# Optimization experiments

Hardware: AMD Instinct MI355X
Metric: run time of the kernel (lower is better)

Reference implementation:

```python
import jax, jax.numpy as jnp
import numpy as np

N = 50000
E = 1600000
SI, SO, VI, VO, H, SVOD = 128, 128, 16, 16, 16, 3
EPS = 1e-8


def _safe_norm(x, axis, keepdims=False):
    return jnp.sqrt(jnp.sum(x * x, axis=axis, keepdims=keepdims) + EPS)


def setup_inputs() -> dict:
    key = jax.random.key(0)
    ks = jax.random.split(key, 13)

    def lin(k, fan_in, shape):
        b = 1.0 / np.sqrt(fan_in)
        return jax.random.uniform(k, shape, jnp.float32, -b, b)

    merged_dim = H + SI + 3 * SVOD  # 153
    return {
        "s": jax.random.normal(ks[0], (N, SI), jnp.float32),
        "v": jax.random.normal(ks[1], (N, VI, 3), jnp.float32),
        "frames": jax.random.normal(ks[2], (E, 3, 3), jnp.float32),
        "W_vd": lin(ks[3], VI, (VI, H)),            # vector_down (no bias)
        "W_vdf": lin(ks[4], VI, (VI, SVOD)),        # vector_down_frames (no bias)
        "W_so": lin(ks[5], merged_dim, (merged_dim, SO)),  # scalar_out
        "b_so": lin(ks[6], merged_dim, (SO,)),
        "W_vu": lin(ks[7], H, (H, VO)),             # vector_up (no bias)
        "W_vosf": lin(ks[8], SO, (SO, 3 * SVOD)),   # vector_out_scale_frames
        "b_vosf": lin(ks[9], SO, (3 * SVOD,)),
        "W_vuf": lin(ks[10], SVOD, (SVOD, VO)),     # vector_up_frames (no bias)
        "edge_index": jax.random.randint(ks[11], (2, E), 0, N, jnp.int32),
        "node_inputs": 1,
    }


def reference(s, v, frames, W_vd, W_vdf, W_so, b_so, W_vu, W_vosf, b_vosf, W_vuf, edge_index, node_inputs):
    # node_inputs is assumed truthy (node-wise GCP): gather by source node, scatter-mean back.
    row = edge_index[0]
    deg = jax.ops.segment_sum(jnp.ones((E,), s.dtype), row, num_segments=N)
    inv_deg = 1.0 / jnp.maximum(deg, 1.0)

    v_pre = jnp.swapaxes(v, -1, -2)                 # [N, 3, VI]
    vh = v_pre @ W_vd                                # [N, 3, H]
    vnorm = _safe_norm(vh, axis=-2)                  # [N, H]
    vdf = v_pre @ W_vdf                              # [N, 3, SVOD]

    # scalarize: project gathered source-node vectors onto per-edge frames, scatter-mean
    local = jnp.einsum('eij,ejc->eic', frames, vdf[row])       # [E, 3, SVOD]
    local9 = jnp.swapaxes(local, -1, -2).reshape(E, 3 * SVOD)  # [E, 9]
    sh = jax.ops.segment_sum(local9, row, num_segments=N) * inv_deg[:, None]  # [N, 9]

    merged = jnp.concatenate([s, vnorm, sh], axis=-1)          # [N, SI+H+9]
    scalar_rep = merged @ W_so + b_so                           # [N, SO]

    # vector path with frame gate
    vr = jnp.swapaxes(vh @ W_vu, -1, -2)                        # [N, VO, 3]
    gate = jax.nn.sigmoid(scalar_rep) @ W_vosf + b_vosf         # [N, 9]
    # vectorize: expand gate scalars back into vectors via frames, scatter-mean
    g = gate[row].reshape(E, 3, 3)
    gv_e = jnp.einsum('eji,ejk->eik', g, frames)                # [E, 3, 3]
    gv = jax.ops.segment_sum(gv_e, row, num_segments=N) * inv_deg[:, None, None]  # [N, 3, 3]
    gvr = jnp.swapaxes(jnp.swapaxes(gv, -1, -2) @ W_vuf, -1, -2)  # [N, VO, 3]
    vr = vr * jax.nn.sigmoid(_safe_norm(gvr, axis=-1, keepdims=True))

    return jax.nn.relu(scalar_rep), vr
```

## Files before the change

kernel.cpp:

```cpp
#include <hip/hip_runtime.h>

#define N_NODES 50000
#define N_EDGES 1600000
#define NPB     16
#define NCHAIN  16
#define KSTR    168
#define EPSV    1e-8f

typedef float f32x4 __attribute__((ext_vector_type(4)));
typedef short s16x8 __attribute__((ext_vector_type(8)));

struct f4u { float a, b, c, d; };

__device__ __forceinline__ float sigmoidf_(float x) { return 1.0f / (1.0f + __expf(-x)); }
__device__ __forceinline__ short f2bf(float x) {
    unsigned u = __float_as_uint(x);
    unsigned r = (u + 0x7FFFu + ((u >> 16) & 1u)) >> 16;
    return (short)r;
}
__device__ __forceinline__ float bf2f(short h) {
    return __uint_as_float(((unsigned)(unsigned short)h) << 16);
}

__global__ __launch_bounds__(256) void init_kernel(
    const float* __restrict__ W_so, short* __restrict__ WThi, short* __restrict__ WTlo,
    int* __restrict__ head) {
    int i = blockIdx.x * 256 + threadIdx.x;
    if (i < 128 * 160) {
        int o = i / 160, k = i - o * 160;
        float w = (k < 153) ? W_so[k * 128 + o] : 0.0f;
        short hh = f2bf(w);
        WThi[i] = hh;
        WTlo[i] = f2bf(w - bf2f(hh));
    }
    if (i < N_NODES * NCHAIN) head[i] = -1;
}

__global__ __launch_bounds__(256) void bucket_fat_kernel(
    const int* __restrict__ row,
    const float* __restrict__ frames,
    int* __restrict__ head,
    float* __restrict__ pay) {
    int e = blockIdx.x * 256 + threadIdx.x;
    if (e >= N_EDGES) return;
    int r = row[e];
    int prev = atomicExch(&head[r * NCHAIN + (e & (NCHAIN - 1))], e);
    const float* f = frames + (size_t)e * 9;
    const f4u* fp = (const f4u*)f;
    f4u x = fp[0];
    f4u y = fp[1];
    float z8 = f[8];
    float4* dst = (float4*)(pay + (size_t)e * 16);
    dst[0] = make_float4(x.a, x.b, x.c, x.d);
    dst[1] = make_float4(y.a, y.b, y.c, y.d);
    dst[2] = make_float4(z8, __int_as_float(prev), 0.0f, 0.0f);
}

__global__ __launch_bounds__(256) void bucket_thin_kernel(
    const int* __restrict__ row,
    int* __restrict__ head,
    int* __restrict__ nxt) {
    int e = blockIdx.x * 256 + threadIdx.x;
    if (e >= N_EDGES) return;
    int r = row[e];
    int prev = atomicExch(&head[r * NCHAIN + (e & (NCHAIN - 1))], e);
    nxt[e] = prev;
}

template<int FAT>
__global__ __launch_bounds__(256) void node_kernel(
    const float* __restrict__ s,
    const float* __restrict__ v,
    const float* __restrict__ fr,
    const float* __restrict__ W_vd,
    const float* __restrict__ W_vdf,
    const short* __restrict__ WThi,
    const short* __restrict__ WTlo,
    const float* __restrict__ b_so,
    const float* __restrict__ W_vu,
    const float* __restrict__ W_vosf,
    const float* __restrict__ b_vosf,
    const float* __restrict__ W_vuf,
    const int* __restrict__ head,
    const int* __restrict__ nxt,
    float* __restrict__ out0,
    float* __restrict__ out1)
{
    __shared__ __align__(16) short AL[2][NPB][KSTR];
    __shared__ float vL[NPB][48];
    __shared__ float vhL[NPB][3][16];
    __shared__ float FbarL[NPB][9];
    __shared__ float gateL[NPB][12];

    float (*sigL)[128] = (float (*)[128])&AL[0][0][0];

    const int t = threadIdx.x;
    const int base = blockIdx.x * NPB;
    const int nn = t >> 4, h = t & 15;
    const int n = base + nn;

    int e = head[(size_t)n * NCHAIN + h];

#pragma unroll
    for (int r = 0; r < 3; r++) vL[nn][h * 3 + r] = v[(size_t)n * 48 + h * 3 + r];
    {
        const float4* sp4 = (const float4*)(s + (size_t)n * 128 + h * 8);
        float4 s0 = sp4[0], s1 = sp4[1];
        float sv[8] = {s0.x, s0.y, s0.z, s0.w, s1.x, s1.y, s1.z, s1.w};
        s16x8 shi, slo;
#pragma unroll
        for (int j = 0; j < 8; j++) {
            short hh = f2bf(sv[j]);
            shi[j] = hh;
            slo[j] = f2bf(sv[j] - bf2f(hh));
        }
        *(s16x8*)&AL[0][nn][h * 8] = shi;
        *(s16x8*)&AL[1][nn][h * 8] = slo;
    }

    float fs[10];
#pragma unroll
    for (int k = 0; k < 10; k++) fs[k] = 0.f;
    {
        if (FAT) {
            while (e >= 0) {
                const float4* p = (const float4*)(fr + (size_t)e * 16);
                float4 c2 = p[2];
                float4 c0 = p[0];
                float4 c1 = p[1];
                int en = __float_as_int(c2.y);
                fs[0] += c0.x; fs[1] += c0.y; fs[2] += c0.z; fs[3] += c0.w;
                fs[4] += c1.x; fs[5] += c1.y; fs[6] += c1.z; fs[7] += c1.w;
                fs[8] += c2.x;
                fs[9] += 1.0f;
                e = en;
            }
        } else {
            while (e >= 0) {
                int en = nxt[e];
                const float* f = fr + (size_t)e * 9;
                const f4u* fp = (const f4u*)f;
                f4u x = fp[0];
                f4u y = fp[1];
                float z8 = f[8];
                fs[0] += x.a; fs[1] += x.b; fs[2] += x.c; fs[3] += x.d;
                fs[4] += y.a; fs[5] += y.b; fs[6] += y.c; fs[7] += y.d;
                fs[8] += z8;
                fs[9] += 1.0f;
                e = en;
            }
        }
#pragma unroll
        for (int m = 1; m < 16; m <<= 1) {
#pragma unroll
            for (int k = 0; k < 10; k++) fs[k] += __shfl_xor(fs[k], m);
        }
        if (h < 9) {
            float inv = 1.0f / fmaxf(fs[9], 1.0f);
            FbarL[nn][h] = fs[h] * inv;
        }
    }
    __syncthreads();

    {
        float vh0 = 0.f, vh1 = 0.f, vh2 = 0.f;
#pragma unroll
        for (int i = 0; i < 16; i++) {
            float w = W_vd[i * 16 + h];
            vh0 += vL[nn][i * 3 + 0] * w;
            vh1 += vL[nn][i * 3 + 1] * w;
            vh2 += vL[nn][i * 3 + 2] * w;
        }
        vhL[nn][0][h] = vh0; vhL[nn][1][h] = vh1; vhL[nn][2][h] = vh2;
        float vn = sqrtf(vh0 * vh0 + vh1 * vh1 + vh2 * vh2 + EPSV);
        short hh = f2bf(vn);
        AL[0][nn][128 + h] = hh;
        AL[1][nn][128 + h] = f2bf(vn - bf2f(hh));
        if (h < 9) {
            const int c = h / 3, i = h % 3;
            const float inv = 1.0f / fmaxf(fs[9], 1.0f);
            float a = 0.f;
#pragma unroll
            for (int j = 0; j < 3; j++) {
                float vd = 0.f;
#pragma unroll
                for (int ii = 0; ii < 16; ii++) vd += vL[nn][ii * 3 + j] * W_vdf[ii * 3 + c];
                a += (fs[i * 3 + j] * inv) * vd;
            }
            short hs = f2bf(a);
            AL[0][nn][144 + h] = hs;
            AL[1][nn][144 + h] = f2bf(a - bf2f(hs));
        } else {
            AL[0][nn][144 + h] = 0;
            AL[1][nn][144 + h] = 0;
        }
    }
    __syncthreads();

    {
        const int w = t >> 6;
        const int lane = t & 63;
        const int quad = lane >> 4;
        const int col = lane & 15;
        const int o0 = w * 32 + col, o1 = o0 + 16;
        f32x4 acc0 = (f32x4){0.f, 0.f, 0.f, 0.f};
        f32x4 acc1 = (f32x4){0.f, 0.f, 0.f, 0.f};
#pragma unroll
        for (int kk = 0; kk < 5; kk++) {
            const int krow = kk * 32 + quad * 8;
            s16x8 ahi = *(const s16x8*)&AL[0][col][krow];
            s16x8 alo = *(const s16x8*)&AL[1][col][krow];
            s16x8 b0h = *(const s16x8*)&WThi[o0 * 160 + krow];
            s16x8 b0l = *(const s16x8*)&WTlo[o0 * 160 + krow];
            s16x8 b1h = *(const s16x8*)&WThi[o1 * 160 + krow];
            s16x8 b1l = *(const s16x8*)&WTlo[o1 * 160 + krow];
            acc0 = __builtin_amdgcn_mfma_f32_16x16x32_bf16(ahi, b0h, acc0, 0, 0, 0);
            acc0 = __builtin_amdgcn_mfma_f32_16x16x32_bf16(ahi, b0l, acc0, 0, 0, 0);
            acc0 = __builtin_amdgcn_mfma_f32_16x16x32_bf16(alo, b0h, acc0, 0, 0, 0);
            acc1 = __builtin_amdgcn_mfma_f32_16x16x32_bf16(ahi, b1h, acc1, 0, 0, 0);
            acc1 = __builtin_amdgcn_mfma_f32_16x16x32_bf16(ahi, b1l, acc1, 0, 0, 0);
            acc1 = __builtin_amdgcn_mfma_f32_16x16x32_bf16(alo, b1h, acc1, 0, 0, 0);
        }
        __syncthreads();
        {
            float b0 = b_so[o0], b1 = b_so[o1];
#pragma unroll
            for (int r = 0; r < 4; r++) {
                int nl = quad * 4 + r;
                float v0 = acc0[r] + b0;
                float v1 = acc1[r] + b1;
                out0[(size_t)(base + nl) * 128 + o0] = fmaxf(v0, 0.0f);
                out0[(size_t)(base + nl) * 128 + o1] = fmaxf(v1, 0.0f);
                sigL[nl][o0] = sigmoidf_(v0);
                sigL[nl][o1] = sigmoidf_(v1);
            }
        }
    }
    __syncthreads();

    {
        const float* sp = &sigL[nn][h * 8];
        float4 s0 = *(const float4*)sp;
        float4 s1 = *(const float4*)(sp + 4);
        float sv[8] = {s0.x, s0.y, s0.z, s0.w, s1.x, s1.y, s1.z, s1.w};
        float p[9];
#pragma unroll
        for (int k = 0; k < 9; k++) p[k] = 0.f;
#pragma unroll
        for (int i = 0; i < 8; i++) {
            int o = h * 8 + i;
#pragma unroll
            for (int k = 0; k < 9; k++) p[k] += sv[i] * W_vosf[o * 9 + k];
        }
#pragma unroll
        for (int m = 1; m < 16; m <<= 1) {
#pragma unroll
            for (int k = 0; k < 9; k++) p[k] += __shfl_xor(p[k], m);
        }
        if (h < 9) gateL[nn][h] = p[h] + b_vosf[h];
    }
    __syncthreads();

    {
        int o = h;
        float gv[9];
#pragma unroll
        for (int i = 0; i < 3; i++)
#pragma unroll
            for (int kk = 0; kk < 3; kk++) {
                float a = 0.f;
#pragma unroll
                for (int j = 0; j < 3; j++) a += gateL[nn][j * 3 + i] * FbarL[nn][j * 3 + kk];
                gv[i * 3 + kk] = a;
            }
        float gvr[3];
#pragma unroll
        for (int kk = 0; kk < 3; kk++) {
            float a = 0.f;
#pragma unroll
            for (int i = 0; i < 3; i++) a += gv[i * 3 + kk] * W_vuf[i * 16 + o];
            gvr[kk] = a;
        }
        float gn2 = sqrtf(gvr[0] * gvr[0] + gvr[1] * gvr[1] + gvr[2] * gvr[2] + EPSV);
        float sg = sigmoidf_(gn2);
#pragma unroll
        for (int c = 0; c < 3; c++) {
            float a = 0.f;
#pragma unroll
            for (int h2 = 0; h2 < 16; h2++) a += vhL[nn][c][h2] * W_vu[h2 * 16 + o];
            out1[(size_t)n * 48 + o * 3 + c] = a * sg;
        }
    }
}

extern "C" void kernel_launch(void* const* d_in, const int* in_sizes, int n_in,
                              void* d_out, int out_size, void* d_ws, size_t ws_size,
                              hipStream_t stream) {
    const float* s      = (const float*)d_in[0];
    const float* v      = (const float*)d_in[1];
    const float* frames = (const float*)d_in[2];
    const float* W_vd   = (const float*)d_in[3];
    const float* W_vdf  = (const float*)d_in[4];
    const float* W_so   = (const float*)d_in[5];
    const float* b_so   = (const float*)d_in[6];
    const float* W_vu   = (const float*)d_in[7];
    const float* W_vosf = (const float*)d_in[8];
    const float* b_vosf = (const float*)d_in[9];
    const float* W_vuf  = (const float*)d_in[10];
    const int* edge_index = (const int*)d_in[11];

    const size_t head_b = (size_t)N_NODES * NCHAIN * sizeof(int);
    const size_t wt_b   = (size_t)128 * 160 * sizeof(short);
    const size_t pay_off = head_b + 2 * wt_b;
    int*   head = (int*)d_ws;
    short* WThi = (short*)((char*)d_ws + head_b);
    short* WTlo = WThi + 128 * 160;
    float* out0 = (float*)d_out;
    float* out1 = out0 + (size_t)N_NODES * 128;

    const size_t fat_need = pay_off + (size_t)N_EDGES * 64;
    init_kernel<<<(N_NODES * NCHAIN + 255) / 256, 256, 0, stream>>>(W_so, WThi, WTlo, head);

    if (ws_size >= fat_need) {
        float* pay = (float*)((char*)d_ws + pay_off);
        bucket_fat_kernel<<<(N_EDGES + 255) / 256, 256, 0, stream>>>(edge_index, frames, head, pay);
        node_kernel<1><<<N_NODES / NPB, 256, 0, stream>>>(
            s, v, pay, W_vd, W_vdf, WThi, WTlo, b_so, W_vu, W_vosf, b_vosf, W_vuf,
            head, (const int*)nullptr, out0, out1);
    } else {
        int* nxt = (int*)((char*)d_ws + pay_off);
        bucket_thin_kernel<<<(N_EDGES + 255) / 256, 256, 0, stream>>>(edge_index, head, nxt);
        node_kernel<0><<<N_NODES / NPB, 256, 0, stream>>>(
            s, v, frames, W_vd, W_vdf, WThi, WTlo, b_so, W_vu, W_vosf, b_vosf, W_vuf,
            head, nxt, out0, out1);
    }
}
```

Measured before the change: 279.6 us.

## Bucket edge frames into per-node fixed-capacity slots instead of linked chains

Adds a CSR-like bucketing path: each edge atomically claims a slot in a per-node array of capacity up to 64 and writes its 9 frame values there. Edges beyond capacity fall back to linked-list chains. The node kernel then reads slots with coalesced strided access instead of serial pointer chasing, and derives the degree from the counter. This removes dependent-load latency in the aggregation, at the cost of a more contended per-node atomic counter and a larger padded workspace.

Result: slower. 307.5 us (+10.0%).

```diff
diff --git a/kernel.cpp b/kernel.cpp
--- a/kernel.cpp
+++ b/kernel.cpp
@@ -24,7 +24,7 @@
 
 __global__ __launch_bounds__(256) void init_kernel(
     const float* __restrict__ W_so, short* __restrict__ WThi, short* __restrict__ WTlo,
-    int* __restrict__ head) {
+    int* __restrict__ p0, int* __restrict__ p1, int mode) {
     int i = blockIdx.x * 256 + threadIdx.x;
     if (i < 128 * 160) {
         int o = i / 160, k = i - o * 160;
@@ -33,7 +33,39 @@
         WThi[i] = hh;
         WTlo[i] = f2bf(w - bf2f(hh));
     }
-    if (i < N_NODES * NCHAIN) head[i] = -1;
+    if (mode == 2) {
+        if (i < N_NODES) p0[i] = 0;
+        if (i < N_NODES * NCHAIN) p1[i] = -1;
+    } else {
+        if (i < N_NODES * NCHAIN) p0[i] = -1;
+    }
+}
+
+__global__ __launch_bounds__(256) void bucket_csr_kernel(
+    const int* __restrict__ row,
+    const float* __restrict__ frames,
+    int* __restrict__ cnt,
+    int* __restrict__ head2,
+    int* __restrict__ nxt_ovf,
+    float* __restrict__ pay,
+    int cap) {
+    int e = blockIdx.x * 256 + threadIdx.x;
+    if (e >= N_EDGES) return;
+    int r = row[e];
+    int lidx = atomicAdd(&cnt[r], 1);
+    if (lidx < cap) {
+        const float* f = frames + (size_t)e * 9;
+        f4u x = ((const f4u*)f)[0];
+        f4u y = ((const f4u*)f)[1];
+        float z8 = f[8];
+        float* dst = pay + ((size_t)r * cap + lidx) * 12;
+        *(float4*)dst       = make_float4(x.a, x.b, x.c, x.d);
+        *(float4*)(dst + 4) = make_float4(y.a, y.b, y.c, y.d);
+        *(float4*)(dst + 8) = make_float4(z8, 0.0f, 0.0f, 0.0f);
+    } else {
+        int prev = atomicExch(&head2[r * NCHAIN + (e & (NCHAIN - 1))], e);
+        nxt_ovf[e] = prev;
+    }
 }
 
 __global__ __launch_bounds__(256) void bucket_fat_kernel(
@@ -46,9 +78,8 @@
     int r = row[e];
     int prev = atomicExch(&head[r * NCHAIN + (e & (NCHAIN - 1))], e);
     const float* f = frames + (size_t)e * 9;
-    const f4u* fp = (const f4u*)f;
-    f4u x = fp[0];
-    f4u y = fp[1];
+    f4u x = ((const f4u*)f)[0];
+    f4u y = ((const f4u*)f)[1];
     float z8 = f[8];
     float4* dst = (float4*)(pay + (size_t)e * 16);
     dst[0] = make_float4(x.a, x.b, x.c, x.d);
@@ -67,11 +98,12 @@
     nxt[e] = prev;
 }
 
-template<int FAT>
+template<int MODE>
 __global__ __launch_bounds__(256) void node_kernel(
     const float* __restrict__ s,
     const float* __restrict__ v,
     const float* __restrict__ fr,
+    const float* __restrict__ frames_raw,
     const float* __restrict__ W_vd,
     const float* __restrict__ W_vdf,
     const short* __restrict__ WThi,
@@ -81,8 +113,10 @@
     const float* __restrict__ W_vosf,
     const float* __restrict__ b_vosf,
     const float* __restrict__ W_vuf,
-    const int* __restrict__ head,
+    const int* __restrict__ cnt_or_head,
+    const int* __restrict__ head2,
     const int* __restrict__ nxt,
+    int cap,
     float* __restrict__ out0,
     float* __restrict__ out1)
 {
@@ -99,7 +133,9 @@
     const int nn = t >> 4, h = t & 15;
     const int n = base + nn;
 
-    int e = head[(size_t)n * NCHAIN + h];
+    int e0;
+    if (MODE == 2) e0 = cnt_or_head[n];
+    else           e0 = cnt_or_head[(size_t)n * NCHAIN + h];
 
 #pragma unroll
     for (int r = 0; r < 3; r++) vL[nn][h * 3 + r] = v[(size_t)n * 48 + h * 3 + r];
@@ -121,8 +157,40 @@
     float fs[10];
 #pragma unroll
     for (int k = 0; k < 10; k++) fs[k] = 0.f;
-    {
-        if (FAT) {
+    float invdeg;
+    {
+        if (MODE == 2) {
+            const int cn = e0;
+            const int lim = cn < cap ? cn : cap;
+            for (int slot = h; slot < lim; slot += 16) {
+                const float* pp = fr + ((size_t)n * cap + slot) * 12;
+                float4 c0 = *(const float4*)pp;
+                float4 c1 = *(const float4*)(pp + 4);
+                float f8 = pp[8];
+                fs[0] += c0.x; fs[1] += c0.y; fs[2] += c0.z; fs[3] += c0.w;
+                fs[4] += c1.x; fs[5] += c1.y; fs[6] += c1.z; fs[7] += c1.w;
+                fs[8] += f8;
+            }
+            int e2 = head2[(size_t)n * NCHAIN + h];
+            while (e2 >= 0) {
+                int en = nxt[e2];
+                const float* f = frames_raw + (size_t)e2 * 9;
+                f4u x = ((const f4u*)f)[0];
+                f4u y = ((const f4u*)f)[1];
+                float z8 = f[8];
+                fs[0] += x.a; fs[1] += x.b; fs[2] += x.c; fs[3] += x.d;
+                fs[4] += y.a; fs[5] += y.b; fs[6] += y.c; fs[7] += y.d;
+                fs[8] += z8;
+                e2 = en;
+            }
+#pragma unroll
+            for (int m = 1; m < 16; m <<= 1) {
+#pragma unroll
+                for (int k = 0; k < 9; k++) fs[k] += __shfl_xor(fs[k], m);
+            }
+            invdeg = 1.0f / fmaxf((float)cn, 1.0f);
+        } else if (MODE == 1) {
+            int e = e0;
             while (e >= 0) {
                 const float4* p = (const float4*)(fr + (size_t)e * 16);
                 float4 c2 = p[2];
@@ -135,13 +203,19 @@
                 fs[9] += 1.0f;
                 e = en;
             }
+#pragma unroll
+            for (int m = 1; m < 16; m <<= 1) {
+#pragma unroll
+                for (int k = 0; k < 10; k++) fs[k] += __shfl_xor(fs[k], m);
+            }
+            invdeg = 1.0f / fmaxf(fs[9], 1.0f);
         } else {
+            int e = e0;
             while (e >= 0) {
                 int en = nxt[e];
                 const float* f = fr + (size_t)e * 9;
-                const f4u* fp = (const f4u*)f;
-                f4u x = fp[0];
-                f4u y = fp[1];
+                f4u x = ((const f4u*)f)[0];
+                f4u y = ((const f4u*)f)[1];
                 float z8 = f[8];
                 fs[0] += x.a; fs[1] += x.b; fs[2] += x.c; fs[3] += x.d;
                 fs[4] += y.a; fs[5] += y.b; fs[6] += y.c; fs[7] += y.d;
@@ -149,16 +223,14 @@
                 fs[9] += 1.0f;
                 e = en;
             }
-        }
-#pragma unroll
-        for (int m = 1; m < 16; m <<= 1) {
-#pragma unroll
-            for (int k = 0; k < 10; k++) fs[k] += __shfl_xor(fs[k], m);
-        }
-        if (h < 9) {
-            float inv = 1.0f / fmaxf(fs[9], 1.0f);
-            FbarL[nn][h] = fs[h] * inv;
-        }
+#pragma unroll
+            for (int m = 1; m < 16; m <<= 1) {
+#pragma unroll
+                for (int k = 0; k < 10; k++) fs[k] += __shfl_xor(fs[k], m);
+            }
+            invdeg = 1.0f / fmaxf(fs[9], 1.0f);
+        }
+        if (h < 9) FbarL[nn][h] = fs[h] * invdeg;
     }
     __syncthreads();
 
@@ -178,14 +250,13 @@
         AL[1][nn][128 + h] = f2bf(vn - bf2f(hh));
         if (h < 9) {
             const int c = h / 3, i = h % 3;
-            const float inv = 1.0f / fmaxf(fs[9], 1.0f);
             float a = 0.f;
 #pragma unroll
             for (int j = 0; j < 3; j++) {
                 float vd = 0.f;
 #pragma unroll
                 for (int ii = 0; ii < 16; ii++) vd += vL[nn][ii * 3 + j] * W_vdf[ii * 3 + c];
-                a += (fs[i * 3 + j] * inv) * vd;
+                a += (fs[i * 3 + j] * invdeg) * vd;
             }
             short hs = f2bf(a);
             AL[0][nn][144 + h] = hs;
@@ -309,29 +380,60 @@
     const float* W_vuf  = (const float*)d_in[10];
     const int* edge_index = (const int*)d_in[11];
 
-    const size_t head_b = (size_t)N_NODES * NCHAIN * sizeof(int);
-    const size_t wt_b   = (size_t)128 * 160 * sizeof(short);
-    const size_t pay_off = head_b + 2 * wt_b;
-    int*   head = (int*)d_ws;
-    short* WThi = (short*)((char*)d_ws + head_b);
-    short* WTlo = WThi + 128 * 160;
     float* out0 = (float*)d_out;
     float* out1 = out0 + (size_t)N_NODES * 128;
 
-    const size_t fat_need = pay_off + (size_t)N_EDGES * 64;
-    init_kernel<<<(N_NODES * NCHAIN + 255) / 256, 256, 0, stream>>>(W_so, WThi, WTlo, head);
-
-    if (ws_size >= fat_need) {
-        float* pay = (float*)((char*)d_ws + pay_off);
-        bucket_fat_kernel<<<(N_EDGES + 255) / 256, 256, 0, stream>>>(edge_index, frames, head, pay);
+    const size_t wt_b    = (size_t)128 * 160 * sizeof(short);
+    const size_t cnt_b   = (size_t)N_NODES * sizeof(int);
+    const size_t head2_b = (size_t)N_NODES * NCHAIN * sizeof(int);
+    const size_t novf_b  = (size_t)N_EDGES * sizeof(int);
+    const size_t csr_base = cnt_b + head2_b + 2 * wt_b + novf_b;
+    long cap = 0;
+    if (ws_size > csr_base)
+        cap = (long)((ws_size - csr_base) / ((size_t)N_NODES * 48));
+    if (cap > 64) cap = 64;
+
+    const size_t head_b  = (size_t)N_NODES * NCHAIN * sizeof(int);
+    const size_t fat_off = head_b + 2 * wt_b;
+    const size_t fat_need = fat_off + (size_t)N_EDGES * 64;
+
+    if (cap >= 32) {
+        int*   cnt   = (int*)d_ws;
+        int*   head2 = (int*)((char*)d_ws + cnt_b);
+        short* WThi  = (short*)((char*)d_ws + cnt_b + head2_b);
+        short* WTlo  = WThi + 128 * 160;
+        int*   novf  = (int*)((char*)d_ws + cnt_b + head2_b + 2 * wt_b);
+        float* pay   = (float*)((char*)d_ws + csr_base);
+        init_kernel<<<(N_NODES * NCHAIN + 255) / 256, 256, 0, stream>>>(
+            W_so, WThi, WTlo, cnt, head2, 2);
+        bucket_csr_kernel<<<(N_EDGES + 255) / 256, 256, 0, stream>>>(
+            edge_index, frames, cnt, head2, novf, pay, (int)cap);
+        node_kernel<2><<<N_NODES / NPB, 256, 0, stream>>>(
+            s, v, pay, frames, W_vd, W_vdf, WThi, WTlo, b_so, W_vu, W_vosf, b_vosf, W_vuf,
+            cnt, head2, novf, (int)cap, out0, out1);
+    } else if (ws_size >= fat_need) {
+        int*   head = (int*)d_ws;
+        short* WThi = (short*)((char*)d_ws + head_b);
+        short* WTlo = WThi + 128 * 160;
+        float* pay  = (float*)((char*)d_ws + fat_off);
+        init_kernel<<<(N_NODES * NCHAIN + 255) / 256, 256, 0, stream>>>(
+            W_so, WThi, WTlo, head, (int*)nullptr, 1);
+        bucket_fat_kernel<<<(N_EDGES + 255) / 256, 256, 0, stream>>>(
+            edge_index, frames, head, pay);
         node_kernel<1><<<N_NODES / NPB, 256, 0, stream>>>(
-            s, v, pay, W_vd, W_vdf, WThi, WTlo, b_so, W_vu, W_vosf, b_vosf, W_vuf,
-            head, (const int*)nullptr, out0, out1);
+            s, v, pay, frames, W_vd, W_vdf, WThi, WTlo, b_so, W_vu, W_vosf, b_vosf, W_vuf,
+            head, (const int*)nullptr, (const int*)nullptr, 0, out0, out1);
     } else {
-        int* nxt = (int*)((char*)d_ws + pay_off);
-        bucket_thin_kernel<<<(N_EDGES + 255) / 256, 256, 0, stream>>>(edge_index, head, nxt);
+        int*   head = (int*)d_ws;
+        short* WThi = (short*)((char*)d_ws + head_b);
+        short* WTlo = WThi + 128 * 160;
+        int*   nxt  = (int*)((char*)d_ws + fat_off);
+        init_kernel<<<(N_NODES * NCHAIN + 255) / 256, 256, 0, stream>>>(
+            W_so, WThi, WTlo, head, (int*)nullptr, 1);
+        bucket_thin_kernel<<<(N_EDGES + 255) / 256, 256, 0, stream>>>(
+            edge_index, head, nxt);
         node_kernel<0><<<N_NODES / NPB, 256, 0, stream>>>(
-            s, v, frames, W_vd, W_vdf, WThi, WTlo, b_so, W_vu, W_vosf, b_vosf, W_vuf,
-            head, nxt, out0, out1);
-    }
-}
+            s, v, frames, frames, W_vd, W_vdf, WThi, WTlo, b_so, W_vu, W_vosf, b_vosf, W_vuf,
+            head, (const int*)nullptr, nxt, 0, out0, out1);
+    }
+}
```
